# Kernel optimization log

Measured on AMD Instinct MI355X. Metric: run time of the kernel, lower is better.

Reference implementation:

```python
import jax, jax.numpy as jnp
import numpy as np

N_NODES = 50000
N_EDGES = 800000
IN_CH, HID_CH, OUT_CH = 128, 128, 64


def _gcn_conv(x, W, b, src, dst, n):
    """PyG GCNConv: self-loops + symmetric norm + linear + scatter-add + bias."""
    loop = jnp.arange(n, dtype=src.dtype)
    src_sl = jnp.concatenate([src, loop])  # [E+N]
    dst_sl = jnp.concatenate([dst, loop])
    # degree computed on edges incl. self-loops (edge weight 1)
    deg = jax.ops.segment_sum(jnp.ones_like(dst_sl, dtype=x.dtype), dst_sl,
                              num_segments=n)
    dinv = jnp.where(deg > 0, jax.lax.rsqrt(deg), 0.0)
    norm = dinv[src_sl] * dinv[dst_sl]  # [E+N]
    xw = x @ W  # [N, F_out]
    msg = xw[src_sl] * norm[:, None]  # gather + scale, [E+N, F_out]
    out = jax.ops.segment_sum(msg, dst_sl, num_segments=n)
    return out + b


def setup_inputs() -> dict:
    key = jax.random.key(0)
    ks = jax.random.split(key, 5)
    x = jax.random.normal(ks[0], (N_NODES, IN_CH), dtype=jnp.float32)
    edge_index = jax.random.randint(ks[1], (2, N_EDGES), 0, N_NODES, dtype=jnp.int64)
    s1 = 1.0 / np.sqrt(IN_CH)
    s2 = 1.0 / np.sqrt(HID_CH)
    W1 = jax.random.normal(ks[2], (IN_CH, HID_CH), dtype=jnp.float32) * s1
    W2 = jax.random.normal(ks[3], (HID_CH, HID_CH), dtype=jnp.float32) * s2
    W3 = jax.random.normal(ks[4], (HID_CH, OUT_CH), dtype=jnp.float32) * s2
    return {
        "x": x, "edge_index": edge_index,
        "W1": W1, "b1": jnp.zeros((HID_CH,), jnp.float32),
        "W2": W2, "b2": jnp.zeros((HID_CH,), jnp.float32),
        "W3": W3, "b3": jnp.zeros((OUT_CH,), jnp.float32),
    }


def reference(x, edge_index, W1, b1, W2, b2, W3, b3):
    n = x.shape[0]
    src, dst = edge_index[0], edge_index[1]
    # dropout(p=0.6) is identity in eval mode
    h = jax.nn.relu(_gcn_conv(x, W1, b1, src, dst, n))
    h = jax.nn.relu(_gcn_conv(h, W2, b2, src, dst, n))
    out = _gcn_conv(h, W3, b3, src, dst, n)
    return out
```

## Files before the change

kernel.cpp:

```cpp
#include <hip/hip_runtime.h>
#include <cstdint>

#define CAP 32768
#define CHUNK 2048

typedef __attribute__((ext_vector_type(8))) short bf8_t;
typedef __attribute__((ext_vector_type(4))) float f4_t;
typedef __attribute__((ext_vector_type(2))) float f2_t;

__device__ __forceinline__ uint32_t f_to_bf(float f) {
    union { float f; uint32_t u; } v; v.f = f;
    uint32_t u = v.u;
    return (u + 0x7fffu + ((u >> 16) & 1u)) >> 16;
}
__device__ __forceinline__ float bf_to_f(uint32_t h) {
    union { uint32_t u; float f; } v; v.u = h << 16; return v.f;
}
__device__ __forceinline__ f2_t bfpair(uint32_t u) {
    union { uint32_t u; float f; } a, b;
    a.u = u << 16; b.u = u & 0xffff0000u;
    f2_t r; r[0] = a.f; r[1] = b.f; return r;
}
__device__ __forceinline__ void fma8pk(f2_t* acc, uint4 u, float d) {
    f2_t dd; dd[0] = d; dd[1] = d;
    acc[0] += bfpair(u.x) * dd;
    acc[1] += bfpair(u.y) * dd;
    acc[2] += bfpair(u.z) * dd;
    acc[3] += bfpair(u.w) * dd;
}

__device__ __forceinline__ int detect64(const int* __restrict__ e32) {
    return (e32[1] | e32[3] | e32[5] | e32[7]) == 0;
}
__device__ __forceinline__ int edge_at(const void* edges, int is64, int idx) {
    if (is64) return (int)((const long long*)edges)[idx];
    return ((const int*)edges)[idx];
}

__global__ __launch_bounds__(256) void prep_kernel(
    const float* __restrict__ W1, const float* __restrict__ W2,
    const float* __restrict__ W3,
    uint16_t* w1h, uint16_t* w1l, uint16_t* w2h, uint16_t* w2l,
    uint16_t* w3h, uint16_t* w3l, int* __restrict__ bucket_cur) {
    if (blockIdx.x == 160) {
        if (threadIdx.x < 64) bucket_cur[threadIdx.x] = threadIdx.x * CAP;
        return;
    }
    int idx = blockIdx.x * 256 + threadIdx.x;
    const float* W; uint16_t* oh; uint16_t* ol; int FOUT; int e;
    if (idx < 16384)      { W = W1; oh = w1h; ol = w1l; FOUT = 128; e = idx; }
    else if (idx < 32768) { W = W2; oh = w2h; ol = w2l; FOUT = 128; e = idx - 16384; }
    else                  { W = W3; oh = w3h; ol = w3l; FOUT = 64;  e = idx - 32768; }
    int j = e & 7;
    int lane = (e >> 3) & 63;
    int rem = e >> 9;
    int NT = FOUT >> 4;
    int nt = rem % NT, kc = rem / NT;
    int k = kc * 32 + ((lane >> 4) << 3) + j;
    int c = nt * 16 + (lane & 15);
    float v = W[(size_t)k * FOUT + c];
    uint32_t h = f_to_bf(v);
    uint32_t l = f_to_bf(v - bf_to_f(h));
    oh[e] = (uint16_t)h;
    ol[e] = (uint16_t)l;
}

__device__ __forceinline__ void gemm1_body(
    const float* __restrict__ A, const uint16_t* __restrict__ Wfhi,
    const uint16_t* __restrict__ Wflo, uint16_t* __restrict__ Yout,
    int n, int cp, int tile0, int tstride, int lane) {
    constexpr int NT = 8, NTW = 2;
    int ntiles = (n + 15) >> 4;
    bf8_t wh[NTW][4], wl[NTW][4];
#pragma unroll
    for (int t = 0; t < NTW; t++) {
        int nt = cp * NTW + t;
#pragma unroll
        for (int kc = 0; kc < 4; kc++) {
            size_t b = ((size_t)(kc * NT + nt) * 64 + lane) * 8;
            wh[t][kc] = *(const bf8_t*)&Wfhi[b];
            wl[t][kc] = *(const bf8_t*)&Wflo[b];
        }
    }
    int row_in = lane & 15;
    int koff = (lane >> 4) << 3;
    int colb = lane & 15;
    int rq = (lane >> 4) << 2;
    for (int tile = tile0; tile < ntiles; tile += tstride) {
        int R = tile << 4;
        int arow = R + row_in; if (arow >= n) arow = n - 1;
        const float* ap = A + (size_t)arow * 128 + koff;
        bf8_t ah[4], al[4];
#pragma unroll
        for (int kc = 0; kc < 4; kc++) {
            float4 pv = *(const float4*)(ap + kc * 32);
            float4 qv = *(const float4*)(ap + kc * 32 + 4);
            float vv[8] = {pv.x, pv.y, pv.z, pv.w, qv.x, qv.y, qv.z, qv.w};
#pragma unroll
            for (int j = 0; j < 8; j++) {
                uint32_t h = f_to_bf(vv[j]);
                ah[kc][j] = (short)h;
                al[kc][j] = (short)f_to_bf(vv[j] - bf_to_f(h));
            }
        }
        f4_t acc[NTW];
#pragma unroll
        for (int t = 0; t < NTW; t++) acc[t] = (f4_t){0.f, 0.f, 0.f, 0.f};
#pragma unroll
        for (int kc = 0; kc < 4; kc++) {
#pragma unroll
            for (int t = 0; t < NTW; t++) {
                acc[t] = __builtin_amdgcn_mfma_f32_16x16x32_bf16(ah[kc], wh[t][kc], acc[t], 0, 0, 0);
                acc[t] = __builtin_amdgcn_mfma_f32_16x16x32_bf16(ah[kc], wl[t][kc], acc[t], 0, 0, 0);
                acc[t] = __builtin_amdgcn_mfma_f32_16x16x32_bf16(al[kc], wh[t][kc], acc[t], 0, 0, 0);
            }
        }
#pragma unroll
        for (int t = 0; t < NTW; t++) {
            int c = (cp * NTW + t) * 16 + colb;
#pragma unroll
            for (int r = 0; r < 4; r++) {
                int row = R + rq + r;
                if (row < n)
                    Yout[(size_t)row * 128 + c] = (uint16_t)f_to_bf(acc[t][r]);
            }
        }
    }
}

__global__ __launch_bounds__(256) void scatter_gemm1_kernel(
    const void* __restrict__ ei, int* __restrict__ bucket_cur,
    int2* __restrict__ buckets, int E, int sbcnt,
    const float* __restrict__ x, const uint16_t* __restrict__ w1h,
    const uint16_t* __restrict__ w1l, uint16_t* __restrict__ y1, int n) {
    int tid = threadIdx.x;
    if ((int)blockIdx.x < sbcnt) {
        __shared__ int cnt[64];
        int base = blockIdx.x * CHUNK;
        int is64 = detect64((const int*)ei);
        if (tid < 64) cnt[tid] = 0;
        __syncthreads();
        int dloc[8];
#pragma unroll
        for (int it = 0; it < 8; it++) {
            int i = base + it * 256 + tid;
            int d = (i < E) ? edge_at(ei, is64, E + i) : -1;
            dloc[it] = d;
            if (d >= 0) atomicAdd(&cnt[d >> 10], 1);
        }
        __syncthreads();
        if (tid < 64) {
            int v = cnt[tid];
            cnt[tid] = atomicAdd(&bucket_cur[tid], v);
        }
        __syncthreads();
#pragma unroll
        for (int it = 0; it < 8; it++) {
            int i = base + it * 256 + tid;
            if (dloc[it] >= 0) {
                int s = edge_at(ei, is64, i);
                int p = atomicAdd(&cnt[dloc[it] >> 10], 1);
                buckets[p] = make_int2(s, dloc[it]);
            }
        }
    } else {
        int lane = tid & 63, wid = tid >> 6;
        gemm1_body(x, w1h, w1l, y1, n, wid, blockIdx.x - sbcnt,
                   gridDim.x - sbcnt, lane);
    }
}

__global__ __launch_bounds__(512) void csr_local_kernel(
    const int2* __restrict__ buckets, const int* __restrict__ bucket_cur,
    int* __restrict__ row_ptr, int* __restrict__ bsum, float* __restrict__ dinv, int n) {
    __shared__ int cnt[1024];
    __shared__ int sb[1024];
    int b = blockIdx.x, tid = threadIdx.x;
    int base = b << 10;
    int lim = min(1024, n - base);
    if (lim <= 0) { if (tid == 0) bsum[b] = 0; return; }
    int ecnt = bucket_cur[b] - b * CAP;
    const int2* ebase = buckets + (size_t)b * CAP;
    for (int i = tid; i < 1024; i += 512) cnt[i] = 0;
    __syncthreads();
    for (int i = tid; i < ecnt; i += 512)
        atomicAdd(&cnt[ebase[i].y - base], 1);
    __syncthreads();
    for (int i = tid; i < lim; i += 512)
        dinv[base + i] = rsqrtf((float)(cnt[i] + 1));
    __syncthreads();
    int* a = cnt; int* s = sb;
    for (int st = 1; st < 1024; st <<= 1) {
        for (int i = tid; i < 1024; i += 512)
            s[i] = a[i] + ((i >= st) ? a[i - st] : 0);
        __syncthreads();
        int* t = a; a = s; s = t;
    }
    for (int i = tid; i < lim; i += 512)
        row_ptr[base + i] = (i > 0) ? a[i - 1] : 0;
    if (tid == 0) bsum[b] = a[1023];
}

__global__ __launch_bounds__(512) void fill_bucket_kernel(
    const int2* __restrict__ buckets, const int* __restrict__ bucket_cur,
    int* __restrict__ row_ptr, const int* __restrict__ bsum,
    int* __restrict__ col, int n, int nbuck) {
    __shared__ int cur[1024];
    __shared__ int s_bo;
    int b = blockIdx.x, tid = threadIdx.x;
    int base = b << 10;
    int lim = min(1024, n - base);
    if (lim <= 0) return;
    if (tid < 64) {
        int lane = tid;
        int v = (lane < nbuck) ? bsum[lane] : 0;
        int incl = v;
#pragma unroll
        for (int off = 1; off < 64; off <<= 1) {
            int t = __shfl_up(incl, off);
            if (lane >= off) incl += t;
        }
        int tot = __shfl(incl, nbuck - 1);
        int bo = (b > 0) ? __shfl(incl, b - 1) : 0;
        if (lane == 0) {
            s_bo = bo;
            if (b == nbuck - 1) row_ptr[n] = tot;
        }
    }
    __syncthreads();
    int ecnt = bucket_cur[b] - b * CAP;
    const int2* ebase = buckets + (size_t)b * CAP;
    int bo = s_bo;
    for (int i = tid; i < lim; i += 512) {
        int v = row_ptr[base + i] + bo;
        row_ptr[base + i] = v;
        cur[i] = v;
    }
    __syncthreads();
    for (int i = tid; i < ecnt; i += 512) {
        int2 e = ebase[i];
        int p = atomicAdd(&cur[e.y - base], 1);
        col[p] = e.x;
    }
}

template <int FOUT, bool SRC_SCALE>
__global__ __launch_bounds__(256) void agg_gemm_kernel(
    const uint16_t* __restrict__ Yin, const int* __restrict__ row_ptr,
    const int* __restrict__ col, const float* __restrict__ dinv,
    const float* __restrict__ bias,
    const uint16_t* __restrict__ Wfhi, const uint16_t* __restrict__ Wflo,
    uint16_t* __restrict__ Yout, int n) {
    __shared__ uint4 hs4[16 * 17];
    __shared__ uint4 ls4[16 * 17];
    int tid = threadIdx.x, wid = tid >> 6, lane = tid & 63;
    int base = blockIdx.x * 16;
    int g = lane & 15, j = lane >> 4;
    const uint4* Y4 = (const uint4*)Yin;

    float4 bb0 = *(const float4*)&bias[g * 8];
    float4 bb1 = *(const float4*)&bias[g * 8 + 4];
    float bb[8] = {bb0.x, bb0.y, bb0.z, bb0.w, bb1.x, bb1.y, bb1.z, bb1.w};

    for (int q = 0; q < 4; q++) {
        int r = wid * 4 + q, node = base + r;
        uint4 ph = (uint4){0, 0, 0, 0}, pl = (uint4){0, 0, 0, 0};
        if (node < n) {
            float di = dinv[node];
            f2_t aA[4] = {}, aB[4] = {};
            {
                float sd = (j == 0) ? (SRC_SCALE ? di : 1.f) : 0.f;
                uint4 su = Y4[(size_t)node * 16 + g];
                fma8pk(aA, su, sd);
            }
            int start = row_ptr[node], end = row_ptr[node + 1];
            for (int b = start; b < end; b += 64) {
                int cnt = min(64, end - b);
                int sv = (b + lane < end) ? col[b + lane] : 0;
                float dv = SRC_SCALE ? dinv[sv] : 1.f;
                for (int k = 0; k < cnt; k += 8) {
                    int iA = k + j, iB = k + 4 + j;
                    int sA = __shfl(sv, iA & 63);
                    int sB = __shfl(sv, iB & 63);
                    float dA, dB;
                    if (SRC_SCALE) {
                        dA = (iA < cnt) ? __shfl(dv, iA & 63) : 0.f;
                        dB = (iB < cnt) ? __shfl(dv, iB & 63) : 0.f;
                    } else {
                        dA = (iA < cnt) ? 1.f : 0.f;
                        dB = (iB < cnt) ? 1.f : 0.f;
                    }
                    uint4 uA = Y4[(size_t)sA * 16 + g];
                    uint4 uB = Y4[(size_t)sB * 16 + g];
                    fma8pk(aA, uA, dA);
                    fma8pk(aB, uB, dB);
                }
            }
            float o[8];
#pragma unroll
            for (int i = 0; i < 4; i++) {
                o[2 * i]     = aA[i][0] + aB[i][0];
                o[2 * i + 1] = aA[i][1] + aB[i][1];
            }
#pragma unroll
            for (int t = 0; t < 8; t++) o[t] += __shfl_xor(o[t], 16);
#pragma unroll
            for (int t = 0; t < 8; t++) o[t] += __shfl_xor(o[t], 32);
            uint32_t hh[8];
#pragma unroll
            for (int t = 0; t < 8; t++) {
                o[t] = fmaxf(o[t] * di + bb[t], 0.f);
                hh[t] = f_to_bf(o[t]);
            }
            ph = (uint4){hh[0] | (hh[1] << 16), hh[2] | (hh[3] << 16),
                         hh[4] | (hh[5] << 16), hh[6] | (hh[7] << 16)};
            uint32_t ll[8];
#pragma unroll
            for (int t = 0; t < 8; t++) ll[t] = f_to_bf(o[t] - bf_to_f(hh[t]));
            pl = (uint4){ll[0] | (ll[1] << 16), ll[2] | (ll[3] << 16),
                         ll[4] | (ll[5] << 16), ll[6] | (ll[7] << 16)};
        }
        if (j == 0) {
            hs4[r * 17 + g] = ph;
            ls4[r * 17 + g] = pl;
        }
    }
    __syncthreads();

    const uint16_t* hs = (const uint16_t*)hs4;
    const uint16_t* ls = (const uint16_t*)ls4;
    constexpr int NT = FOUT / 16;
    constexpr int NTW = NT / 4;
    constexpr int LDW = 136;
    int cp = wid;
    bf8_t wh[NTW][4], wl[NTW][4];
#pragma unroll
    for (int t = 0; t < NTW; t++) {
        int nt = cp * NTW + t;
#pragma unroll
        for (int kc = 0; kc < 4; kc++) {
            size_t b = ((size_t)(kc * NT + nt) * 64 + lane) * 8;
            wh[t][kc] = *(const bf8_t*)&Wfhi[b];
            wl[t][kc] = *(const bf8_t*)&Wflo[b];
        }
    }
    int koff = (lane >> 4) << 3;
    int colb = lane & 15;
    int rq = (lane >> 4) << 2;
    bf8_t ah[4], al[4];
#pragma unroll
    for (int kc = 0; kc < 4; kc++) {
        ah[kc] = *(const bf8_t*)(hs + (lane & 15) * LDW + koff + kc * 32);
        al[kc] = *(const bf8_t*)(ls + (lane & 15) * LDW + koff + kc * 32);
    }
    f4_t acc[NTW];
#pragma unroll
    for (int t = 0; t < NTW; t++) acc[t] = (f4_t){0.f, 0.f, 0.f, 0.f};
#pragma unroll
    for (int kc = 0; kc < 4; kc++) {
#pragma unroll
        for (int t = 0; t < NTW; t++) {
            acc[t] = __builtin_amdgcn_mfma_f32_16x16x32_bf16(ah[kc], wh[t][kc], acc[t], 0, 0, 0);
            acc[t] = __builtin_amdgcn_mfma_f32_16x16x32_bf16(ah[kc], wl[t][kc], acc[t], 0, 0, 0);
            acc[t] = __builtin_amdgcn_mfma_f32_16x16x32_bf16(al[kc], wh[t][kc], acc[t], 0, 0, 0);
        }
    }
#pragma unroll
    for (int t = 0; t < NTW; t++) {
        int c = (cp * NTW + t) * 16 + colb;
#pragma unroll
        for (int r = 0; r < 4; r++) {
            int row = base + rq + r;
            if (row < n) {
                float v = acc[t][r] * dinv[row];
                Yout[(size_t)row * FOUT + c] = (uint16_t)f_to_bf(v);
            }
        }
    }
}

__global__ __launch_bounds__(256) void agg_final_kernel(
    const uint16_t* __restrict__ Y, const int* __restrict__ row_ptr,
    const int* __restrict__ col, const float* __restrict__ dinv,
    const float* __restrict__ bias, float* __restrict__ out, int n) {
    int w = blockIdx.x * 4 + (threadIdx.x >> 6);
    int lane = threadIdx.x & 63;
    if (w >= n) return;
    int g = lane & 7, j = lane >> 3;
    const uint4* Y4 = (const uint4*)Y;
    float4 bb0 = *(const float4*)&bias[g * 8];
    float4 bb1 = *(const float4*)&bias[g * 8 + 4];
    float bb[8] = {bb0.x, bb0.y, bb0.z, bb0.w, bb1.x, bb1.y, bb1.z, bb1.w};

    f2_t aA[4] = {}, aB[4] = {};
    {
        uint4 su = Y4[(size_t)w * 8 + g];
        fma8pk(aA, su, (j == 0) ? 1.f : 0.f);
    }
    int start = row_ptr[w], end = row_ptr[w + 1];
    for (int b = start; b < end; b += 64) {
        int cnt = min(64, end - b);
        int sv = (b + lane < end) ? col[b + lane] : 0;
        for (int k = 0; k < cnt; k += 16) {
            int iA = k + j, iB = k + 8 + j;
            int sA = __shfl(sv, iA & 63);
            int sB = __shfl(sv, iB & 63);
            float dA = (iA < cnt) ? 1.f : 0.f;
            float dB = (iB < cnt) ? 1.f : 0.f;
            uint4 uA = Y4[(size_t)sA * 8 + g];
            uint4 uB = Y4[(size_t)sB * 8 + g];
            fma8pk(aA, uA, dA);
            fma8pk(aB, uB, dB);
        }
    }
    float o[8];
#pragma unroll
    for (int i = 0; i < 4; i++) {
        o[2 * i]     = aA[i][0] + aB[i][0];
        o[2 * i + 1] = aA[i][1] + aB[i][1];
    }
#pragma unroll
    for (int t = 0; t < 8; t++) o[t] += __shfl_xor(o[t], 8);
#pragma unroll
    for (int t = 0; t < 8; t++) o[t] += __shfl_xor(o[t], 16);
#pragma unroll
    for (int t = 0; t < 8; t++) o[t] += __shfl_xor(o[t], 32);
    float di = dinv[w];
#pragma unroll
    for (int t = 0; t < 8; t++) o[t] = o[t] * di + bb[t];
    if (j == 0) {
        float4 o0 = {o[0], o[1], o[2], o[3]};
        float4 o1 = {o[4], o[5], o[6], o[7]};
        *(float4*)&out[(size_t)w * 64 + g * 8] = o0;
        *(float4*)&out[(size_t)w * 64 + g * 8 + 4] = o1;
    }
}

extern "C" void kernel_launch(void* const* d_in, const int* in_sizes, int n_in,
                              void* d_out, int out_size, void* d_ws, size_t ws_size,
                              hipStream_t stream) {
    const float* x  = (const float*)d_in[0];
    const void*  ei = d_in[1];
    const float* W1 = (const float*)d_in[2];
    const float* b1 = (const float*)d_in[3];
    const float* W2 = (const float*)d_in[4];
    const float* b2 = (const float*)d_in[5];
    const float* W3 = (const float*)d_in[6];
    const float* b3 = (const float*)d_in[7];
    int n = in_sizes[0] / 128;
    int E = in_sizes[1] / 2;
    int nbuck = (n + 1023) >> 10;

    char* p = (char*)d_ws;
    auto carve = [&](size_t bytes) {
        char* r = p;
        p += (bytes + 255) & ~(size_t)255;
        return r;
    };
    float*    dinv       = (float*)carve((size_t)n * 4);
    int*      row_ptr    = (int*)carve((size_t)(n + 1) * 4);
    int*      bsum       = (int*)carve(64 * 4);
    int*      bucket_cur = (int*)carve(64 * 4);
    int*      col        = (int*)carve((size_t)E * 4);
    int2*     buckets    = (int2*)carve((size_t)64 * CAP * 8);
    uint16_t* y1         = (uint16_t*)carve((size_t)n * 128 * 2);
    uint16_t* y2         = (uint16_t*)carve((size_t)n * 128 * 2);
    uint16_t* y3         = (uint16_t*)carve((size_t)n * 64 * 2);
    uint16_t* w1h        = (uint16_t*)carve(128 * 128 * 2);
    uint16_t* w1l        = (uint16_t*)carve(128 * 128 * 2);
    uint16_t* w2h        = (uint16_t*)carve(128 * 128 * 2);
    uint16_t* w2l        = (uint16_t*)carve(128 * 128 * 2);
    uint16_t* w3h        = (uint16_t*)carve(128 * 64 * 2);
    uint16_t* w3l        = (uint16_t*)carve(128 * 64 * 2);

    int sbcnt = (E + CHUNK - 1) / CHUNK;
    int fb = (n + 15) / 16;

    prep_kernel<<<161, 256, 0, stream>>>(W1, W2, W3, w1h, w1l, w2h, w2l,
                                         w3h, w3l, bucket_cur);
    scatter_gemm1_kernel<<<sbcnt + 782, 256, 0, stream>>>(
        ei, bucket_cur, buckets, E, sbcnt, x, w1h, w1l, y1, n);
    csr_local_kernel<<<nbuck, 512, 0, stream>>>(buckets, bucket_cur, row_ptr, bsum, dinv, n);
    fill_bucket_kernel<<<nbuck, 512, 0, stream>>>(buckets, bucket_cur, row_ptr, bsum,
                                                  col, n, nbuck);
    agg_gemm_kernel<128, true><<<fb, 256, 0, stream>>>(
        y1, row_ptr, col, dinv, b1, w2h, w2l, y2, n);
    agg_gemm_kernel<64, false><<<fb, 256, 0, stream>>>(
        y2, row_ptr, col, dinv, b2, w3h, w3l, y3, n);
    agg_final_kernel<<<(n + 3) / 4, 256, 0, stream>>>(
        y3, row_ptr, col, dinv, b3, (float*)d_out, n);
}
```

Before: 246.6 us.

## Use 1024-thread blocks with one wave per node in fused agg-GEMM kernels

The fused aggregate+GEMM kernel now launches 16 waves per block, so each wave aggregates a single node instead of looping over four. The MFMA stage is split so each of the first NT waves computes one 16-column tile, and the remaining waves sit idle there. The source degree scale is now loaded per gathered edge from dinv instead of once per lane and shuffled, which adds scattered loads. The goal is more wave-level parallelism to hide gather latency, at the cost of large blocks, idle waves during the GEMM and extra dinv reads.

```diff
diff --git a/kernel.cpp b/kernel.cpp
--- a/kernel.cpp
+++ b/kernel.cpp
@@ -245,7 +245,7 @@
 }
 
 template <int FOUT, bool SRC_SCALE>
-__global__ __launch_bounds__(256) void agg_gemm_kernel(
+__global__ __launch_bounds__(1024) void agg_gemm_kernel(
     const uint16_t* __restrict__ Yin, const int* __restrict__ row_ptr,
     const int* __restrict__ col, const float* __restrict__ dinv,
     const float* __restrict__ bias,
@@ -262,117 +262,97 @@
     float4 bb1 = *(const float4*)&bias[g * 8 + 4];
     float bb[8] = {bb0.x, bb0.y, bb0.z, bb0.w, bb1.x, bb1.y, bb1.z, bb1.w};
 
-    for (int q = 0; q < 4; q++) {
-        int r = wid * 4 + q, node = base + r;
-        uint4 ph = (uint4){0, 0, 0, 0}, pl = (uint4){0, 0, 0, 0};
-        if (node < n) {
-            float di = dinv[node];
-            f2_t aA[4] = {}, aB[4] = {};
-            {
-                float sd = (j == 0) ? (SRC_SCALE ? di : 1.f) : 0.f;
-                uint4 su = Y4[(size_t)node * 16 + g];
-                fma8pk(aA, su, sd);
-            }
-            int start = row_ptr[node], end = row_ptr[node + 1];
-            for (int b = start; b < end; b += 64) {
-                int cnt = min(64, end - b);
-                int sv = (b + lane < end) ? col[b + lane] : 0;
-                float dv = SRC_SCALE ? dinv[sv] : 1.f;
-                for (int k = 0; k < cnt; k += 8) {
-                    int iA = k + j, iB = k + 4 + j;
-                    int sA = __shfl(sv, iA & 63);
-                    int sB = __shfl(sv, iB & 63);
-                    float dA, dB;
-                    if (SRC_SCALE) {
-                        dA = (iA < cnt) ? __shfl(dv, iA & 63) : 0.f;
-                        dB = (iB < cnt) ? __shfl(dv, iB & 63) : 0.f;
-                    } else {
-                        dA = (iA < cnt) ? 1.f : 0.f;
-                        dB = (iB < cnt) ? 1.f : 0.f;
-                    }
-                    uint4 uA = Y4[(size_t)sA * 16 + g];
-                    uint4 uB = Y4[(size_t)sB * 16 + g];
-                    fma8pk(aA, uA, dA);
-                    fma8pk(aB, uB, dB);
-                }
-            }
-            float o[8];
-#pragma unroll
-            for (int i = 0; i < 4; i++) {
-                o[2 * i]     = aA[i][0] + aB[i][0];
-                o[2 * i + 1] = aA[i][1] + aB[i][1];
-            }
-#pragma unroll
-            for (int t = 0; t < 8; t++) o[t] += __shfl_xor(o[t], 16);
-#pragma unroll
-            for (int t = 0; t < 8; t++) o[t] += __shfl_xor(o[t], 32);
-            uint32_t hh[8];
-#pragma unroll
-            for (int t = 0; t < 8; t++) {
-                o[t] = fmaxf(o[t] * di + bb[t], 0.f);
-                hh[t] = f_to_bf(o[t]);
-            }
-            ph = (uint4){hh[0] | (hh[1] << 16), hh[2] | (hh[3] << 16),
-                         hh[4] | (hh[5] << 16), hh[6] | (hh[7] << 16)};
-            uint32_t ll[8];
-#pragma unroll
-            for (int t = 0; t < 8; t++) ll[t] = f_to_bf(o[t] - bf_to_f(hh[t]));
-            pl = (uint4){ll[0] | (ll[1] << 16), ll[2] | (ll[3] << 16),
-                         ll[4] | (ll[5] << 16), ll[6] | (ll[7] << 16)};
-        }
-        if (j == 0) {
-            hs4[r * 17 + g] = ph;
-            ls4[r * 17 + g] = pl;
-        }
-    }
-    __syncthreads();
-
-    const uint16_t* hs = (const uint16_t*)hs4;
-    const uint16_t* ls = (const uint16_t*)ls4;
+    int r = wid, node = base + r;
+    uint4 ph = (uint4){0, 0, 0, 0}, pl = (uint4){0, 0, 0, 0};
+    if (node < n) {
+        float di = dinv[node];
+        f2_t aA[4] = {}, aB[4] = {};
+        {
+            float sd = (j == 0) ? (SRC_SCALE ? di : 1.f) : 0.f;
+            uint4 su = Y4[(size_t)node * 16 + g];
+            fma8pk(aA, su, sd);
+        }
+        int start = row_ptr[node], end = row_ptr[node + 1];
+        for (int b = start; b < end; b += 64) {
+            int cnt = min(64, end - b);
+            int sv = (b + lane < end) ? col[b + lane] : 0;
+            for (int k = 0; k < cnt; k += 8) {
+                int iA = k + j, iB = k + 4 + j;
+                int sA = __shfl(sv, iA & 63);
+                int sB = __shfl(sv, iB & 63);
+                float dA = (iA < cnt) ? (SRC_SCALE ? dinv[sA] : 1.f) : 0.f;
+                float dB = (iB < cnt) ? (SRC_SCALE ? dinv[sB] : 1.f) : 0.f;
+                uint4 uA = Y4[(size_t)sA * 16 + g];
+                uint4 uB = Y4[(size_t)sB * 16 + g];
+                fma8pk(aA, uA, dA);
+                fma8pk(aB, uB, dB);
+            }
+        }
+        float o[8];
+#pragma unroll
+        for (int i = 0; i < 4; i++) {
+            o[2 * i]     = aA[i][0] + aB[i][0];
+            o[2 * i + 1] = aA[i][1] + aB[i][1];
+        }
+#pragma unroll
+        for (int t = 0; t < 8; t++) o[t] += __shfl_xor(o[t], 16);
+#pragma unroll
+        for (int t = 0; t < 8; t++) o[t] += __shfl_xor(o[t], 32);
+        uint32_t hh[8];
+#pragma unroll
+        for (int t = 0; t < 8; t++) {
+            o[t] = fmaxf(o[t] * di + bb[t], 0.f);
+            hh[t] = f_to_bf(o[t]);
+        }
+        ph = (uint4){hh[0] | (hh[1] << 16), hh[2] | (hh[3] << 16),
+                     hh[4] | (hh[5] << 16), hh[6] | (hh[7] << 16)};
+        uint32_t ll[8];
+#pragma unroll
+        for (int t = 0; t < 8; t++) ll[t] = f_to_bf(o[t] - bf_to_f(hh[t]));
+        pl = (uint4){ll[0] | (ll[1] << 16), ll[2] | (ll[3] << 16),
+                     ll[4] | (ll[5] << 16), ll[6] | (ll[7] << 16)};
+    }
+    if (j == 0) {
+        hs4[r * 17 + g] = ph;
+        ls4[r * 17 + g] = pl;
+    }
+    __syncthreads();
+
     constexpr int NT = FOUT / 16;
-    constexpr int NTW = NT / 4;
-    constexpr int LDW = 136;
-    int cp = wid;
-    bf8_t wh[NTW][4], wl[NTW][4];
-#pragma unroll
-    for (int t = 0; t < NTW; t++) {
-        int nt = cp * NTW + t;
-#pragma unroll
-        for (int kc = 0; kc < 4; kc++) {
-            size_t b = ((size_t)(kc * NT + nt) * 64 + lane) * 8;
-            wh[t][kc] = *(const bf8_t*)&Wfhi[b];
-            wl[t][kc] = *(const bf8_t*)&Wflo[b];
-        }
-    }
-    int koff = (lane >> 4) << 3;
-    int colb = lane & 15;
-    int rq = (lane >> 4) << 2;
-    bf8_t ah[4], al[4];
-#pragma unroll
-    for (int kc = 0; kc < 4; kc++) {
-        ah[kc] = *(const bf8_t*)(hs + (lane & 15) * LDW + koff + kc * 32);
-        al[kc] = *(const bf8_t*)(ls + (lane & 15) * LDW + koff + kc * 32);
-    }
-    f4_t acc[NTW];
-#pragma unroll
-    for (int t = 0; t < NTW; t++) acc[t] = (f4_t){0.f, 0.f, 0.f, 0.f};
-#pragma unroll
-    for (int kc = 0; kc < 4; kc++) {
-#pragma unroll
-        for (int t = 0; t < NTW; t++) {
-            acc[t] = __builtin_amdgcn_mfma_f32_16x16x32_bf16(ah[kc], wh[t][kc], acc[t], 0, 0, 0);
-            acc[t] = __builtin_amdgcn_mfma_f32_16x16x32_bf16(ah[kc], wl[t][kc], acc[t], 0, 0, 0);
-            acc[t] = __builtin_amdgcn_mfma_f32_16x16x32_bf16(al[kc], wh[t][kc], acc[t], 0, 0, 0);
-        }
-    }
-#pragma unroll
-    for (int t = 0; t < NTW; t++) {
-        int c = (cp * NTW + t) * 16 + colb;
-#pragma unroll
-        for (int r = 0; r < 4; r++) {
-            int row = base + rq + r;
+    if (wid < NT) {
+        const uint16_t* hs = (const uint16_t*)hs4;
+        const uint16_t* ls = (const uint16_t*)ls4;
+        constexpr int LDW = 136;
+        int cp = wid;
+        bf8_t wh[4], wl[4];
+#pragma unroll
+        for (int kc = 0; kc < 4; kc++) {
+            size_t b = ((size_t)(kc * NT + cp) * 64 + lane) * 8;
+            wh[kc] = *(const bf8_t*)&Wfhi[b];
+            wl[kc] = *(const bf8_t*)&Wflo[b];
+        }
+        int koff = (lane >> 4) << 3;
+        int colb = lane & 15;
+        int rq = (lane >> 4) << 2;
+        bf8_t ah[4], al[4];
+#pragma unroll
+        for (int kc = 0; kc < 4; kc++) {
+            ah[kc] = *(const bf8_t*)(hs + (lane & 15) * LDW + koff + kc * 32);
+            al[kc] = *(const bf8_t*)(ls + (lane & 15) * LDW + koff + kc * 32);
+        }
+        f4_t acc = (f4_t){0.f, 0.f, 0.f, 0.f};
+#pragma unroll
+        for (int kc = 0; kc < 4; kc++) {
+            acc = __builtin_amdgcn_mfma_f32_16x16x32_bf16(ah[kc], wh[kc], acc, 0, 0, 0);
+            acc = __builtin_amdgcn_mfma_f32_16x16x32_bf16(ah[kc], wl[kc], acc, 0, 0, 0);
+            acc = __builtin_amdgcn_mfma_f32_16x16x32_bf16(al[kc], wh[kc], acc, 0, 0, 0);
+        }
+        int c = cp * 16 + colb;
+#pragma unroll
+        for (int r4 = 0; r4 < 4; r4++) {
+            int row = base + rq + r4;
             if (row < n) {
-                float v = acc[t][r] * dinv[row];
+                float v = acc[r4] * dinv[row];
                 Yout[(size_t)row * FOUT + c] = (uint16_t)f_to_bf(v);
             }
         }
@@ -483,9 +463,9 @@
     csr_local_kernel<<<nbuck, 512, 0, stream>>>(buckets, bucket_cur, row_ptr, bsum, dinv, n);
     fill_bucket_kernel<<<nbuck, 512, 0, stream>>>(buckets, bucket_cur, row_ptr, bsum,
                                                   col, n, nbuck);
-    agg_gemm_kernel<128, true><<<fb, 256, 0, stream>>>(
+    agg_gemm_kernel<128, true><<<fb, 1024, 0, stream>>>(
         y1, row_ptr, col, dinv, b1, w2h, w2l, y2, n);
-    agg_gemm_kernel<64, false><<<fb, 256, 0, stream>>>(
+    agg_gemm_kernel<64, false><<<fb, 1024, 0, stream>>>(
         y2, row_ptr, col, dinv, b2, w3h, w3l, y3, n);
     agg_final_kernel<<<(n + 3) / 4, 256, 0, stream>>>(
         y3, row_ptr, col, dinv, b3, (float*)d_out, n);
```

Result: no change. 249.9 us (+1.4%).
